# Kernel tuning notes

Hardware: AMD Instinct MI355X
Metric: run time of the kernel (lower is better)

The kernel has to match this reference:

```python
import jax, jax.numpy as jnp
import numpy as np

D_ENC = 640  # encoder feature dim


def setup_inputs() -> dict:
    key = jax.random.key(0)
    k1, k2, k3 = jax.random.split(key, 3)
    B, T, U1 = 8, 256, 65  # U1 = maxU + 1
    D_pred = 640
    V = 1024  # num_outputs + 1
    encoder_out = jax.random.normal(k1, (B, T, D_ENC), dtype=jnp.float32)
    predictor_out = jax.random.normal(k2, (B, U1, D_pred), dtype=jnp.float32)
    W = jax.random.normal(k3, (D_ENC + D_pred, V), dtype=jnp.float32) * 0.02
    b = jnp.zeros((V,), dtype=jnp.float32)
    return {"encoder_out": encoder_out, "predictor_out": predictor_out, "W": W, "b": b}


def reference(encoder_out, predictor_out, W, b):
    # Original: tile enc over U+1, tile pred over T, concat on feature dim, Dense.
    # Mathematically identical: split W into encoder/predictor halves and
    # broadcast-add the two projections (avoids the O(T*U*2D) concat buffer).
    We = W[:D_ENC]   # [D_enc, V]
    Wp = W[D_ENC:]   # [D_pred, V]
    enc_proj = jnp.einsum("btd,dv->btv", encoder_out, We)      # [B, T, V]
    pred_proj = jnp.einsum("bud,dv->buv", predictor_out, Wp)   # [B, U+1, V]
    out = enc_proj[:, :, None, :] + pred_proj[:, None, :, :] + b  # [B, T, U+1, V]
    return out
```

## Files before the change

### kernel.cpp

```cpp
#include <hip/hip_runtime.h>

constexpr int B  = 8;
constexpr int T  = 256;
constexpr int U1 = 65;
constexpr int DK = 640;
constexpr int V  = 1024;

constexpr int M_ENC  = B * T;
constexpr int M_PRED = B * U1;

constexpr int NKS  = DK / 32;
constexpr int RT_E = M_ENC / 16;
constexpr int RT_P = 36;
constexpr int CT   = V / 16;

typedef float  f32x4  __attribute__((ext_vector_type(4)));
typedef short  short8 __attribute__((ext_vector_type(8)));
typedef unsigned short u16x4 __attribute__((ext_vector_type(4)));

__device__ __forceinline__ short f2bf(float f) {
    union { float f; unsigned u; } x; x.f = f;
    unsigned r = x.u + 0x7fffu + ((x.u >> 16) & 1u);
    return (short)(r >> 16);
}
__device__ __forceinline__ f32x4 bf4_to_f32(u16x4 s) {
    f32x4 o;
    union { unsigned u; float f; } x;
    x.u = ((unsigned)s[0]) << 16; o[0] = x.f;
    x.u = ((unsigned)s[1]) << 16; o[1] = x.f;
    x.u = ((unsigned)s[2]) << 16; o[2] = x.f;
    x.u = ((unsigned)s[3]) << 16; o[3] = x.f;
    return o;
}

constexpr int NB_AE = RT_E * NKS * 64 / 256;
constexpr int NB_AP = RT_P * NKS * 64 / 256;
constexpr int NB_BE = CT   * NKS * 64 / 256;
constexpr int NB_BP = NB_BE;

__global__ __launch_bounds__(256) void prep_kernel(
    const float* __restrict__ enc, const float* __restrict__ pred,
    const float* __restrict__ W,
    short* __restrict__ Apack_e, short* __restrict__ Apack_p,
    short* __restrict__ Bpack_e, short* __restrict__ Bpack_p)
{
    const int bid = blockIdx.x;
    const int tid = threadIdx.x;

    if (bid < NB_AE) {
        const int chunk = bid * 256 + tid;
        const int l  = chunk & 63;
        const int ks = (chunk >> 6) % NKS;
        const int rt = chunk / (64 * NKS);
        const int row = rt * 16 + (l & 15);
        const float* src = enc + (size_t)row * DK + ks * 32 + (l >> 4) * 8;
        const f32x4 x = *reinterpret_cast<const f32x4*>(src);
        const f32x4 y = *reinterpret_cast<const f32x4*>(src + 4);
        short8 s;
        s[0]=f2bf(x[0]); s[1]=f2bf(x[1]); s[2]=f2bf(x[2]); s[3]=f2bf(x[3]);
        s[4]=f2bf(y[0]); s[5]=f2bf(y[1]); s[6]=f2bf(y[2]); s[7]=f2bf(y[3]);
        *reinterpret_cast<short8*>(Apack_e + (size_t)chunk * 8) = s;
    } else if (bid < NB_AE + NB_AP) {
        const int chunk = (bid - NB_AE) * 256 + tid;
        const int l  = chunk & 63;
        const int ks = (chunk >> 6) % NKS;
        const int rt = chunk / (64 * NKS);
        const int row = rt * 16 + (l & 15);
        short8 s;
        if (row < M_PRED) {
            const float* src = pred + (size_t)row * DK + ks * 32 + (l >> 4) * 8;
            const f32x4 x = *reinterpret_cast<const f32x4*>(src);
            const f32x4 y = *reinterpret_cast<const f32x4*>(src + 4);
            s[0]=f2bf(x[0]); s[1]=f2bf(x[1]); s[2]=f2bf(x[2]); s[3]=f2bf(x[3]);
            s[4]=f2bf(y[0]); s[5]=f2bf(y[1]); s[6]=f2bf(y[2]); s[7]=f2bf(y[3]);
        } else {
            #pragma unroll
            for (int j = 0; j < 8; ++j) s[j] = 0;
        }
        *reinterpret_cast<short8*>(Apack_p + (size_t)chunk * 8) = s;
    } else {
        const bool isE = (bid < NB_AE + NB_AP + NB_BE);
        const int  base = isE ? (NB_AE + NB_AP) : (NB_AE + NB_AP + NB_BE);
        short* Bp = isE ? Bpack_e : Bpack_p;
        const int kofs = isE ? 0 : DK;
        const int chunk = (bid - base) * 256 + tid;
        const int l  = chunk & 63;
        const int ks = (chunk >> 6) % NKS;
        const int ct = chunk / (64 * NKS);
        const int v  = ct * 16 + (l & 15);
        const int k0 = kofs + ks * 32 + (l >> 4) * 8;
        short8 s;
        #pragma unroll
        for (int j = 0; j < 8; ++j)
            s[j] = f2bf(W[(size_t)(k0 + j) * V + v]);
        *reinterpret_cast<short8*>(Bp + (size_t)chunk * 8) = s;
    }
}

constexpr int NB_GP = (RT_P / 4) * 16;

__global__ __launch_bounds__(256) void gemm_pred_kernel(
    const short* __restrict__ Apack_p, const short* __restrict__ Bpack_p,
    const float* __restrict__ bias, short* __restrict__ pred_proj)
{
    const int rb = blockIdx.x >> 4;
    const int cb = blockIdx.x & 15;

    const int wid  = threadIdx.x >> 6;
    const int lane = threadIdx.x & 63;
    const int wr   = wid >> 1, wc = wid & 1;
    const int m    = lane & 15, g = lane >> 4;

    const int rt0 = rb * 4 + wr * 2;
    const int ct0 = cb * 4 + wc * 2;

    const short* a0p = Apack_p + ((size_t)rt0 * NKS) * 512 + lane * 8;
    const short* a1p = a0p + (size_t)NKS * 512;
    const short* b0p = Bpack_p + ((size_t)ct0 * NKS) * 512 + lane * 8;
    const short* b1p = b0p + (size_t)NKS * 512;

    f32x4 z4; z4[0]=z4[1]=z4[2]=z4[3]=0.f;
    f32x4 acc00 = z4, acc01 = z4, acc10 = z4, acc11 = z4;

    #pragma unroll 4
    for (int ks = 0; ks < NKS; ++ks) {
        const size_t o = (size_t)ks * 512;
        const short8 a0 = *reinterpret_cast<const short8*>(a0p + o);
        const short8 a1 = *reinterpret_cast<const short8*>(a1p + o);
        const short8 b0 = *reinterpret_cast<const short8*>(b0p + o);
        const short8 b1 = *reinterpret_cast<const short8*>(b1p + o);
        acc00 = __builtin_amdgcn_mfma_f32_16x16x32_bf16(a0, b0, acc00, 0, 0, 0);
        acc01 = __builtin_amdgcn_mfma_f32_16x16x32_bf16(a0, b1, acc01, 0, 0, 0);
        acc10 = __builtin_amdgcn_mfma_f32_16x16x32_bf16(a1, b0, acc10, 0, 0, 0);
        acc11 = __builtin_amdgcn_mfma_f32_16x16x32_bf16(a1, b1, acc11, 0, 0, 0);
    }

    #pragma unroll
    for (int nt = 0; nt < 2; ++nt) {
        const int col = (ct0 + nt) * 16 + m;
        const float bv = bias[col];
        #pragma unroll
        for (int mt = 0; mt < 2; ++mt) {
            const f32x4 a = nt ? (mt ? acc11 : acc01) : (mt ? acc10 : acc00);
            #pragma unroll
            for (int q = 0; q < 4; ++q) {
                const int row = (rt0 + mt) * 16 + g * 4 + q;
                if (row < M_PRED)
                    pred_proj[(size_t)row * V + col] = f2bf(a[q] + bv);
            }
        }
    }
}

__global__ __launch_bounds__(256) void fused_kernel(
    const short* __restrict__ Apack_e, const short* __restrict__ Bpack_e,
    const short* __restrict__ pred_proj, float* __restrict__ out)
{
    __shared__ short p_s[U1 * 128];
    __shared__ short e_s[16 * 128];

    const int rt   = blockIdx.x >> 3;
    const int cp   = blockIdx.x & 7;
    const int b    = rt >> 4;
    const int col0 = cp * 128;
    const int tid  = threadIdx.x;

    for (int i = tid; i < U1 * 16; i += 256) {
        const int u = i >> 4;
        const int c = (i & 15) * 8;
        *reinterpret_cast<short8*>(p_s + u * 128 + c) =
            *reinterpret_cast<const short8*>(
                pred_proj + ((size_t)(b * U1 + u)) * V + col0 + c);
    }

    const int wid  = tid >> 6;
    const int lane = tid & 63;
    const int m    = lane & 15, g = lane >> 4;

    const short* ap  = Apack_e + ((size_t)rt * NKS) * 512 + lane * 8;
    const int   ct0  = cp * 8 + wid * 2;
    const short* b0p = Bpack_e + ((size_t)ct0 * NKS) * 512 + lane * 8;
    const short* b1p = b0p + (size_t)NKS * 512;

    f32x4 z4; z4[0]=z4[1]=z4[2]=z4[3]=0.f;
    f32x4 acc0 = z4, acc1 = z4;

    #pragma unroll 4
    for (int ks = 0; ks < NKS; ++ks) {
        const size_t o = (size_t)ks * 512;
        const short8 a  = *reinterpret_cast<const short8*>(ap  + o);
        const short8 b0 = *reinterpret_cast<const short8*>(b0p + o);
        const short8 b1 = *reinterpret_cast<const short8*>(b1p + o);
        acc0 = __builtin_amdgcn_mfma_f32_16x16x32_bf16(a, b0, acc0, 0, 0, 0);
        acc1 = __builtin_amdgcn_mfma_f32_16x16x32_bf16(a, b1, acc1, 0, 0, 0);
    }

    #pragma unroll
    for (int nt = 0; nt < 2; ++nt) {
        const f32x4 a = nt ? acc1 : acc0;
        const int col = wid * 32 + nt * 16 + m;
        #pragma unroll
        for (int q = 0; q < 4; ++q)
            e_s[(g * 4 + q) * 128 + col] = f2bf(a[q]);
    }
    __syncthreads();

    const int c4 = tid & 31;
    const int r8 = tid >> 5;
    const f32x4 e0 = bf4_to_f32(*reinterpret_cast<const u16x4*>(
        e_s + r8 * 128 + c4 * 4));
    const f32x4 e1 = bf4_to_f32(*reinterpret_cast<const u16x4*>(
        e_s + (8 + r8) * 128 + c4 * 4));

    float* o0 = out + ((size_t)(rt * 16 + r8) * U1) * V + col0 + c4 * 4;
    float* o1 = out + ((size_t)(rt * 16 + 8 + r8) * U1) * V + col0 + c4 * 4;

    for (int u = 0; u < U1; ++u) {
        const f32x4 pf = bf4_to_f32(*reinterpret_cast<const u16x4*>(
            p_s + u * 128 + c4 * 4));
        *reinterpret_cast<f32x4*>(o0 + (size_t)u * V) = e0 + pf;
        *reinterpret_cast<f32x4*>(o1 + (size_t)u * V) = e1 + pf;
    }
}

extern "C" void kernel_launch(void* const* d_in, const int* in_sizes, int n_in,
                              void* d_out, int out_size, void* d_ws, size_t ws_size,
                              hipStream_t stream)
{
    const float* enc  = (const float*)d_in[0];
    const float* pred = (const float*)d_in[1];
    const float* W    = (const float*)d_in[2];
    const float* bias = (const float*)d_in[3];
    float* out = (float*)d_out;

    short* Apack_e  = (short*)d_ws;
    short* Apack_p  = Apack_e + (size_t)RT_E * NKS * 512;
    short* Bpack_e  = Apack_p + (size_t)RT_P * NKS * 512;
    short* Bpack_p  = Bpack_e + (size_t)CT * NKS * 512;
    short* pred_proj = Bpack_p + (size_t)CT * NKS * 512;

    prep_kernel<<<NB_AE + NB_AP + NB_BE + NB_BP, 256, 0, stream>>>(
        enc, pred, W, Apack_e, Apack_p, Bpack_e, Bpack_p);

    gemm_pred_kernel<<<NB_GP, 256, 0, stream>>>(
        Apack_p, Bpack_p, bias, pred_proj);

    fused_kernel<<<RT_E * 8, 256, 0, stream>>>(
        Apack_e, Bpack_e, pred_proj, out);
}
```

Measured before the change: 130.0 us.

## Widen fused tile to 256 columns and stream pred_proj from global

The fused kernel now has each block cover 256 output columns instead of 128, so each wave computes four MFMA column tiles that share one A load, and the grid is halved. The shared-memory staging of pred_proj is removed. Each thread instead reads pred_proj rows straight from global memory in batches of eight and writes four output rows per pred row. The aim is to cut redundant A-operand loads, the LDS staging pass and per-block overhead in an output-write-bound kernel. In exchange, each block does more serial work and uses more registers, and with fewer blocks occupancy may drop.

```diff
diff --git a/kernel.cpp b/kernel.cpp
--- a/kernel.cpp
+++ b/kernel.cpp
@@ -152,74 +152,88 @@
     }
 }
 
+constexpr int NB_F = RT_E * 4;
+
 __global__ __launch_bounds__(256) void fused_kernel(
     const short* __restrict__ Apack_e, const short* __restrict__ Bpack_e,
     const short* __restrict__ pred_proj, float* __restrict__ out)
 {
-    __shared__ short p_s[U1 * 128];
-    __shared__ short e_s[16 * 128];
-
-    const int rt   = blockIdx.x >> 3;
-    const int cp   = blockIdx.x & 7;
+    __shared__ short e_s[16 * 256];
+
+    const int rt   = blockIdx.x >> 2;
+    const int cp   = blockIdx.x & 3;
     const int b    = rt >> 4;
-    const int col0 = cp * 128;
+    const int col0 = cp * 256;
     const int tid  = threadIdx.x;
-
-    for (int i = tid; i < U1 * 16; i += 256) {
-        const int u = i >> 4;
-        const int c = (i & 15) * 8;
-        *reinterpret_cast<short8*>(p_s + u * 128 + c) =
-            *reinterpret_cast<const short8*>(
-                pred_proj + ((size_t)(b * U1 + u)) * V + col0 + c);
-    }
 
     const int wid  = tid >> 6;
     const int lane = tid & 63;
     const int m    = lane & 15, g = lane >> 4;
 
-    const short* ap  = Apack_e + ((size_t)rt * NKS) * 512 + lane * 8;
-    const int   ct0  = cp * 8 + wid * 2;
-    const short* b0p = Bpack_e + ((size_t)ct0 * NKS) * 512 + lane * 8;
-    const short* b1p = b0p + (size_t)NKS * 512;
+    const short* ap = Apack_e + ((size_t)rt * NKS) * 512 + lane * 8;
+    const int ct0   = cp * 16 + wid * 4;
+    const short* bp = Bpack_e + ((size_t)ct0 * NKS) * 512 + lane * 8;
 
     f32x4 z4; z4[0]=z4[1]=z4[2]=z4[3]=0.f;
-    f32x4 acc0 = z4, acc1 = z4;
+    f32x4 acc[4];
+    #pragma unroll
+    for (int t = 0; t < 4; ++t) acc[t] = z4;
 
     #pragma unroll 4
     for (int ks = 0; ks < NKS; ++ks) {
         const size_t o = (size_t)ks * 512;
-        const short8 a  = *reinterpret_cast<const short8*>(ap  + o);
-        const short8 b0 = *reinterpret_cast<const short8*>(b0p + o);
-        const short8 b1 = *reinterpret_cast<const short8*>(b1p + o);
-        acc0 = __builtin_amdgcn_mfma_f32_16x16x32_bf16(a, b0, acc0, 0, 0, 0);
-        acc1 = __builtin_amdgcn_mfma_f32_16x16x32_bf16(a, b1, acc1, 0, 0, 0);
-    }
-
-    #pragma unroll
-    for (int nt = 0; nt < 2; ++nt) {
-        const f32x4 a = nt ? acc1 : acc0;
-        const int col = wid * 32 + nt * 16 + m;
+        const short8 a = *reinterpret_cast<const short8*>(ap + o);
+        #pragma unroll
+        for (int t = 0; t < 4; ++t) {
+            const short8 bt = *reinterpret_cast<const short8*>(
+                bp + (size_t)t * NKS * 512 + o);
+            acc[t] = __builtin_amdgcn_mfma_f32_16x16x32_bf16(a, bt, acc[t], 0, 0, 0);
+        }
+    }
+
+    #pragma unroll
+    for (int t = 0; t < 4; ++t) {
+        const int col = wid * 64 + t * 16 + m;
         #pragma unroll
         for (int q = 0; q < 4; ++q)
-            e_s[(g * 4 + q) * 128 + col] = f2bf(a[q]);
+            e_s[(g * 4 + q) * 256 + col] = f2bf(acc[t][q]);
     }
     __syncthreads();
 
-    const int c4 = tid & 31;
-    const int r8 = tid >> 5;
-    const f32x4 e0 = bf4_to_f32(*reinterpret_cast<const u16x4*>(
-        e_s + r8 * 128 + c4 * 4));
-    const f32x4 e1 = bf4_to_f32(*reinterpret_cast<const u16x4*>(
-        e_s + (8 + r8) * 128 + c4 * 4));
-
-    float* o0 = out + ((size_t)(rt * 16 + r8) * U1) * V + col0 + c4 * 4;
-    float* o1 = out + ((size_t)(rt * 16 + 8 + r8) * U1) * V + col0 + c4 * 4;
-
-    for (int u = 0; u < U1; ++u) {
-        const f32x4 pf = bf4_to_f32(*reinterpret_cast<const u16x4*>(
-            p_s + u * 128 + c4 * 4));
-        *reinterpret_cast<f32x4*>(o0 + (size_t)u * V) = e0 + pf;
-        *reinterpret_cast<f32x4*>(o1 + (size_t)u * V) = e1 + pf;
+    const int c4 = tid & 63;
+    const int r4 = tid >> 6;
+
+    f32x4 e[4];
+    #pragma unroll
+    for (int i = 0; i < 4; ++i)
+        e[i] = bf4_to_f32(*reinterpret_cast<const u16x4*>(
+            e_s + (r4 + i * 4) * 256 + c4 * 4));
+
+    const short* p = pred_proj + (size_t)b * U1 * V + col0 + c4 * 4;
+    float* orow[4];
+    #pragma unroll
+    for (int i = 0; i < 4; ++i)
+        orow[i] = out + ((size_t)(rt * 16 + r4 + i * 4) * U1) * V + col0 + c4 * 4;
+
+    for (int u0 = 0; u0 < 64; u0 += 8) {
+        u16x4 pv[8];
+        #pragma unroll
+        for (int j = 0; j < 8; ++j)
+            pv[j] = *reinterpret_cast<const u16x4*>(p + (size_t)(u0 + j) * V);
+        #pragma unroll
+        for (int j = 0; j < 8; ++j) {
+            const f32x4 pf = bf4_to_f32(pv[j]);
+            #pragma unroll
+            for (int i = 0; i < 4; ++i)
+                *reinterpret_cast<f32x4*>(orow[i] + (size_t)(u0 + j) * V) = e[i] + pf;
+        }
+    }
+    {
+        const f32x4 pf = bf4_to_f32(
+            *reinterpret_cast<const u16x4*>(p + (size_t)64 * V));
+        #pragma unroll
+        for (int i = 0; i < 4; ++i)
+            *reinterpret_cast<f32x4*>(orow[i] + (size_t)64 * V) = e[i] + pf;
     }
 }
 
@@ -245,6 +259,6 @@
     gemm_pred_kernel<<<NB_GP, 256, 0, stream>>>(
         Apack_p, Bpack_p, bias, pred_proj);
 
-    fused_kernel<<<RT_E * 8, 256, 0, stream>>>(
+    fused_kernel<<<NB_F, 256, 0, stream>>>(
         Apack_e, Bpack_e, pred_proj, out);
 }
```

After: 144.3 us. +11.0%, slower.
